# Optimization experiments

Hardware: AMD Instinct MI355X
Metric: run time of the kernel (lower is better)

Reference implementation:

```python
import jax, jax.numpy as jnp
import numpy as np

ALPHA, BETA, GAMMA = 1.0, 1.0, 0.7
WIN = 11
C1 = 0.01 ** 2
C2 = 0.03 ** 2


def get_sobel_kernels(n1=1, n2=2, n3=2):
    a = np.asarray
    Sx = a([[[-n1, 0, n1], [-n2, 0, n2], [-n1, 0, n1]],
            [[-n2, 0, n2], [-n3 * n2, 0, n3 * n2], [-n2, 0, n2]],
            [[-n1, 0, n1], [-n2, 0, n2], [-n1, 0, n1]]])
    Sy = a([[[-n1, -n2, -n1], [0, 0, 0], [n1, n2, n1]],
            [[-n2, -n3 * n2, -n2], [0, 0, 0], [n2, n3 * n2, n2]],
            [[-n1, -n2, -n1], [0, 0, 0], [n1, n2, n1]]])
    Sz = a([[[-n1, -n2, -n1], [-n2, -n3 * n2, -n2], [-n1, -n2, -n1]],
            [[0, 0, 0], [0, 0, 0], [0, 0, 0]],
            [[n1, n2, n1], [n2, n3 * n2, n2], [n1, n2, n1]]])
    Sd11 = a([[[0, n1, n2], [-n1, 0, n1], [-n2, -n1, 0]],
              [[0, n2, n2 * n3], [-n2, 0, n2], [-n2 * n3, -n2, 0]],
              [[0, n1, n2], [-n1, 0, n1], [-n2, -n1, 0]]])
    Sd12 = a([[[-n2, -n1, 0], [-n1, 0, n1], [0, n1, n2]],
              [[-n2 * n3, -n2, 0], [-n2, 0, n2], [0, n2, n2 * n3]],
              [[-n2, -n1, 0], [-n1, 0, n1], [0, n1, n2]]])
    Sd21 = Sd11.T
    Sd22 = Sd12.T
    Sd31 = a([-S.T for S in Sd11.T])
    Sd32 = a([S.T for S in Sd12.T])
    return np.stack([Sx, Sy, Sz, Sd11, Sd12, Sd21, Sd22, Sd31, Sd32]).astype(np.float32)

# (9,1,3,3,3) fused sobel bank -- single grouped conv instead of 9 launches
SOBEL_W = jnp.asarray(get_sobel_kernels()[:, None])


def _gauss1d():
    g = jnp.exp(-(jnp.arange(WIN, dtype=jnp.float32) - WIN // 2) ** 2 / (2 * 1.5 ** 2))
    return g / g.sum()

G1D = _gauss1d()


def conv3d(x, w):
    return jax.lax.conv_general_dilated(
        x, w, window_strides=(1, 1, 1), padding='SAME',
        dimension_numbers=('NCDHW', 'OIDHW', 'NCDHW'))


def gauss_filter(x):
    # separable 11-tap gaussian along D, H, W (== full 11^3 window, zero-padded SAME)
    x = conv3d(x, G1D.reshape(1, 1, WIN, 1, 1))
    x = conv3d(x, G1D.reshape(1, 1, 1, WIN, 1))
    x = conv3d(x, G1D.reshape(1, 1, 1, 1, WIN))
    return x


def edge_map(img):
    # GradEdge3D.__call__ with a=1, C=1
    B, C, D, H, W = img.shape
    xp = jnp.pad(img, ((0, 0), (0, 0), (1, 1), (1, 1), (1, 1)), mode='reflect')
    g = conv3d(xp, SOBEL_W)                       # (B, 9, D+2, H+2, W+2)
    gm = jnp.sqrt(jnp.sum((g + 1e-6) ** 2 + 1e-6, axis=1))  # (B, D+2, H+2, W+2)
    gm = gm[:, 1:-1, 1:-1, 1:-1]
    norm = (gm - gm.min()) / (gm.max() - gm.min() + 1e-6)
    return norm.reshape(B, 1, D, H, W)


def ssim_value(pred, target):
    mu_p = gauss_filter(pred)
    mu_t = gauss_filter(target)
    mu_p2, mu_t2, mu_pt = mu_p ** 2, mu_t ** 2, mu_p * mu_t
    sig_p = gauss_filter(pred * pred) - mu_p2
    sig_t = gauss_filter(target * target) - mu_t2
    sig_pt = gauss_filter(pred * target) - mu_pt
    ssim_map = ((2 * mu_pt + C1) * (2 * sig_pt + C2)) / ((mu_p2 + mu_t2 + C1) * (sig_p + sig_t + C2))
    return 1.0 - ssim_map.mean()


def setup_inputs() -> dict:
    key = jax.random.key(0)
    k1, k2 = jax.random.split(key)
    shape = (2, 1, 128, 128, 128)
    return {
        'pred': jax.random.uniform(k1, shape, dtype=jnp.float32),
        'target': jax.random.uniform(k2, shape, dtype=jnp.float32),
    }


def reference(pred, target):
    loss_mse = jnp.mean((pred - target) ** 2)
    loss_ssim = ssim_value(pred, target)
    # GMELoss3D: lam_errors=[(1.0, L1Loss())], reduction='sum'
    loss_gme = 1e-6 + jnp.mean(jnp.abs(edge_map(pred) - edge_map(target)))
    total = ALPHA * loss_mse + BETA * loss_ssim + GAMMA * loss_gme
    return (total, loss_mse, loss_ssim, loss_gme)
```

## Files before the change

### kernel.cpp

```cpp
#include <hip/hip_runtime.h>


#define VOL 4194304
#define HV  2097152

typedef _Float16 h2 __attribute__((ext_vector_type(2)));
typedef _Float16 h4 __attribute__((ext_vector_type(4)));
typedef _Float16 h8 __attribute__((ext_vector_type(8)));

constexpr float GW[11] = {
    0.00102838f, 0.00759876f, 0.03600077f, 0.10936070f, 0.21300554f,
    0.26601173f,
    0.21300554f, 0.10936070f, 0.03600077f, 0.00759876f, 0.00102838f};



__device__ __forceinline__ void wblur_body(
    const float* __restrict__ p, const float* __restrict__ t,
    _Float16* __restrict__ A, double* __restrict__ mseB, const int bidx,
    char* __restrict__ pool, float* __restrict__ redw) {
  float (* __restrict__ sr)[138] = (float (*)[138])pool;
  float (* __restrict__ dr)[138] = (float (*)[138])(pool + 8832);
  const int tid = threadIdx.x;
  const int gbase = bidx << 11;
  if (tid < 160) {
    const int r = tid / 10, j = tid % 10;
    const int c = (j < 5) ? j : (128 + j);
    sr[r][c] = 0.f; dr[r][c] = 0.f;
  }
  float msel = 0.f;
#pragma unroll
  for (int i = 0; i < 8; ++i) {
    const int v = (i << 8) + tid;
    const float pv = p[gbase + v];
    const float tv = t[gbase + v];
    const float sv = pv + tv, dv = pv - tv;
    sr[v >> 7][5 + (v & 127)] = sv;
    dr[v >> 7][5 + (v & 127)] = dv;
    msel += dv * dv;
  }
  __syncthreads();
  h4* __restrict__ A4 = (h4*)A;
#pragma unroll
  for (int i = 0; i < 8; ++i) {
    const int v = (i << 8) + tid;
    const int row = v >> 7, x = v & 127;
    float as = 0.f, ad = 0.f, ass = 0.f, add_ = 0.f;
#pragma unroll
    for (int k = 0; k < 11; ++k) {
      const float w = GW[k];
      const float a = sr[row][x + k];
      const float b = dr[row][x + k];
      const float wa = w * a;
      const float wb = w * b;
      as += wa; ad += wb;
      ass += wa * a; add_ += wb * b;
    }
    h4 o;
    o[0] = (_Float16)as;  o[1] = (_Float16)ad;
    o[2] = (_Float16)ass; o[3] = (_Float16)add_;
    A4[gbase + v] = o;
  }
  redw[tid] = msel;
  __syncthreads();
  for (int s = 128; s > 0; s >>= 1) {
    if (tid < s) redw[tid] += redw[tid + s];
    __syncthreads();
  }
  if (tid == 0) atomicAdd(&mseB[(bidx & 63) << 3], (double)redw[0]);
}

__device__ __forceinline__ void sobel_body(
    const float* __restrict__ p, const float* __restrict__ t,
    _Float16* __restrict__ gmP, _Float16* __restrict__ gmT,
    unsigned int* __restrict__ ui, const int bx, const int by, const int bz,
    char* __restrict__ pool, float* __restrict__ rmin) {
  float* __restrict__ sb   = (float*)pool;
  float* __restrict__ rmax = (float*)(pool + 5184);
  const int tid = threadIdx.x;
  const int tx = tid & 15;
  const int ty = tid >> 4;
  const int x0 = bx << 4;
  const int y0 = by << 4;
  const int vol = bz >> 3;
  const int b   = (bz >> 2) & 1;
  const int z0  = (bz & 3) << 5;
  const float* __restrict__ img = vol ? t : p;
  _Float16* __restrict__ gm = vol ? gmT : gmP;
  const int vb = b << 21;

  const int ly1 = tid / 24, lx1 = tid % 24;
  const bool v1 = (lx1 < 18);
  int gy1 = y0 - 1 + ly1; gy1 = gy1 < 0 ? 1 : (gy1 > 127 ? 126 : gy1);
  int gx1 = x0 - 1 + lx1; gx1 = gx1 < 0 ? 1 : (gx1 > 127 ? 126 : gx1);
  const int off1 = (gy1 << 7) + gx1;
  const int s2i = tid + 256;
  const int ly2 = s2i / 24, lx2 = s2i % 24;
  const bool v2 = (s2i < 432) && (lx2 < 18);
  int gy2 = y0 - 1 + ly2; gy2 = gy2 < 0 ? 1 : (gy2 > 127 ? 126 : gy2);
  int gx2 = x0 - 1 + lx2; gx2 = gx2 < 0 ? 1 : (gx2 > 127 ? 126 : gx2);
  const int off2 = (gy2 << 7) + gx2;
  const int rb = ty * 24 + tx;
  const int gbase = vb + (z0 << 14) + ((y0 + ty) << 7) + (x0 + tx);

  float Y0[7], Y1[7], Y2[7];
  float rv1 = 0.f, rv2 = 0.f;
  float lmin = 3.4e38f, lmax = 0.f;

#define LOADR(ZS) {                                                         \
    const int zc_ = (ZS) > 127 ? 126 : (ZS);                                \
    const int za_ = vb + (zc_ << 14);                                       \
    if (v1) rv1 = img[za_ + off1];                                          \
    if (v2) rv2 = img[za_ + off2]; }

#define WRITELDS(BOFF) {                                                    \
    if (v1) sb[(BOFF) + tid] = rv1;                                         \
    if (v2) sb[(BOFF) + s2i] = rv2; }

#define COMPY(P) {                                                          \
    const int o_ = (P) * 432 + rb;                                          \
    const float r00 = sb[o_],      r01 = sb[o_ + 1],  r02 = sb[o_ + 2];     \
    const float r10 = sb[o_ + 24], r11 = sb[o_ + 25], r12 = sb[o_ + 26];    \
    const float r20 = sb[o_ + 48], r21 = sb[o_ + 49], r22 = sb[o_ + 50];    \
    const float dx0 = r02 - r00, dx1 = r12 - r10, dx2 = r22 - r20;          \
    const float ux0 = r00 + r01 + r02, ux1 = r10 + r11 + r12,               \
                ux2 = r20 + r21 + r22;                                      \
    const float sx0 = ux0 + r01, sx1 = ux1 + r11, sx2 = ux2 + r21;          \
    Y##P[1] = dx0 + dx1 + dx2;                                    \
    Y##P[0] = Y##P[1] + dx1;                                      \
    Y##P[2] = sx2 - sx0;                                          \
    Y##P[4] = sx0 + sx1 + sx2;                                    \
    Y##P[3] = Y##P[4] + sx1;                                      \
    Y##P[5] = ux2 - ux0;                                          \
    Y##P[6] = (ux0 + ux2) + 2.f * ux1; }

#define EMIT(I, P0, P1, P2) {                                               \
    const float E_ = Y##P0[0] + Y##P1[0] + Y##P2[0];                        \
    const float g1 = E_ + Y##P1[0];                                         \
    const float tA = Y##P0[1] + Y##P1[1] + Y##P2[1];                        \
    const float A_ = tA + Y##P1[1];                                         \
    const float D_ = Y##P0[2] + Y##P1[2] + Y##P2[2];                        \
    const float g2 = D_ + Y##P1[2];                                         \
    const float g3 = Y##P2[3] - Y##P0[3];                                   \
    const float C_ = Y##P2[4] - Y##P0[4];                                   \
    const float B_ = (Y##P0[5] + Y##P2[5]) + 2.f * Y##P1[5];                \
    const float F_ = Y##P2[6] - Y##P0[6];                                   \
    const float g4 = A_ - B_, g5 = A_ + B_;                                 \
    const float g6 = C_ - D_, g7 = C_ + D_;                                 \
    const float g8 = E_ - F_, g9 = E_ + F_;                                 \
    float ss_ = 9e-6f, t_;                                                  \
    t_ = g1 + 1e-6f; ss_ = fmaf(t_, t_, ss_);                               \
    t_ = g2 + 1e-6f; ss_ = fmaf(t_, t_, ss_);                               \
    t_ = g3 + 1e-6f; ss_ = fmaf(t_, t_, ss_);                               \
    t_ = g4 + 1e-6f; ss_ = fmaf(t_, t_, ss_);                               \
    t_ = g5 + 1e-6f; ss_ = fmaf(t_, t_, ss_);                               \
    t_ = g6 + 1e-6f; ss_ = fmaf(t_, t_, ss_);                               \
    t_ = g7 + 1e-6f; ss_ = fmaf(t_, t_, ss_);                               \
    t_ = g8 + 1e-6f; ss_ = fmaf(t_, t_, ss_);                               \
    t_ = g9 + 1e-6f; ss_ = fmaf(t_, t_, ss_);                               \
    const _Float16 gh = (_Float16)sqrtf(ss_);                               \
    gm[gbase + ((I) << 14)] = gh;                                           \
    const float gq = (float)gh;                                             \
    lmin = fminf(lmin, gq); lmax = fmaxf(lmax, gq); }

#define BODY(I, P0, P1, P2) {                                               \
    WRITELDS((P2) * 432);                                                   \
    LOADR(z0 + (I) + 2);                                                    \
    __syncthreads();                                                        \
    COMPY(P2);                                                              \
    EMIT(I, P0, P1, P2); }

  {
    const int zp = (z0 == 0) ? 1 : (z0 - 1);
    LOADR(zp);  WRITELDS(0);
    LOADR(z0);  WRITELDS(432);
    __syncthreads();
    COMPY(0);
    COMPY(1);
    LOADR(z0 + 1);
  }
  for (int ii = 0; ii < 30; ii += 3) {
    BODY(ii,     0, 1, 2);
    BODY(ii + 1, 1, 2, 0);
    BODY(ii + 2, 2, 0, 1);
  }
  BODY(30, 0, 1, 2);
  BODY(31, 1, 2, 0);

#undef BODY
#undef EMIT
#undef COMPY
#undef WRITELDS
#undef LOADR

  rmin[tid] = lmin; rmax[tid] = lmax;
  __syncthreads();
  for (int st = 128; st > 0; st >>= 1) {
    if (tid < st) {
      rmin[tid] = fminf(rmin[tid], rmin[tid + st]);
      rmax[tid] = fmaxf(rmax[tid], rmax[tid + st]);
    }
    __syncthreads();
  }
  if (tid == 0) {
    const int bin = (bx + (by << 3) + (bz << 6)) & 63;
    atomicMax(&ui[vol * 1024 + (bin << 4)], ~__float_as_uint(rmin[0]));
    atomicMax(&ui[2048 + vol * 1024 + (bin << 4)], __float_as_uint(rmax[0]));
  }
}

__device__ __forceinline__ void blury_body(
    const _Float16* __restrict__ A, _Float16* __restrict__ B,
    const int z, const int yseg, const int batch) {
  __shared__ h8 s[26][64];
  const int tid = threadIdx.x;
  const int y0 = yseg << 4;
  const h8* __restrict__ Ah = (const h8*)A;
  h8* __restrict__ Bh = (h8*)B;
  const int slice8 = (batch << 20) + (z << 13);
  for (int l = tid; l < 1664; l += 256) {
    const int row = l >> 6, xc = l & 63;
    const int y = y0 - 5 + row;
    h8 v{};
    if ((unsigned)y < 128u) v = Ah[slice8 + (y << 6) + xc];
    s[row][xc] = v;
  }
  __syncthreads();
  const int xc = tid & 63;
  const int yg = tid >> 6;
#pragma unroll
  for (int r = 0; r < 4; ++r) {
    const int yo = (yg << 2) + r;
    h8 acc{};
#pragma unroll
    for (int k = 0; k < 11; ++k) {
      const _Float16 w = (_Float16)GW[k];
      acc += w * s[yo + k][xc];
    }
    Bh[slice8 + ((y0 + yo) << 6) + xc] = acc;
  }
}

__device__ __forceinline__ void edge_body(
    const _Float16* __restrict__ gmP, const _Float16* __restrict__ gmT,
    const unsigned int* __restrict__ ui, double* __restrict__ absB,
    const int bidx, float* __restrict__ rede) {
  unsigned umnp = 0u, umnt = 0u, umxp = 0u, umxt = 0u;
  for (int j = 0; j < 64; ++j) {
    const unsigned a0 = ui[j << 4];
    const unsigned a1 = ui[1024 + (j << 4)];
    const unsigned a2 = ui[2048 + (j << 4)];
    const unsigned a3 = ui[3072 + (j << 4)];
    umnp = umnp > a0 ? umnp : a0;
    umnt = umnt > a1 ? umnt : a1;
    umxp = umxp > a2 ? umxp : a2;
    umxt = umxt > a3 ? umxt : a3;
  }
  const float mnp = __uint_as_float(~umnp);
  const float mnt = __uint_as_float(~umnt);
  const float mxp = __uint_as_float(umxp);
  const float mxt = __uint_as_float(umxt);
  const float scp = 1.f / (mxp - mnp + 1e-6f);
  const float sct = 1.f / (mxt - mnt + 1e-6f);
  const h8* __restrict__ gp = (const h8*)gmP;
  const h8* __restrict__ gt = (const h8*)gmT;
  float lsum = 0.f;
  const int base = bidx << 9;
#pragma unroll
  for (int i = 0; i < 2; ++i) {
    const int idx = base + (i << 8) + threadIdx.x;
    const h8 a = gp[idx];
    const h8 b = gt[idx];
#pragma unroll
    for (int j = 0; j < 8; ++j)
      lsum += fabsf(((float)a[j] - mnp) * scp - ((float)b[j] - mnt) * sct);
  }
  rede[threadIdx.x] = lsum;
  __syncthreads();
  for (int s = 128; s > 0; s >>= 1) {
    if (threadIdx.x < s) rede[threadIdx.x] += rede[threadIdx.x + s];
    __syncthreads();
  }
  if (threadIdx.x == 0)
    atomicAdd(&absB[(bidx & 63) << 3], (double)rede[0]);
}

__global__ __launch_bounds__(256) void k_fused_a(
    const float* __restrict__ p, const float* __restrict__ t,
    _Float16* __restrict__ A, double* __restrict__ mseB,
    _Float16* __restrict__ gmP, _Float16* __restrict__ gmT,
    unsigned int* __restrict__ ui) {
  __shared__ __align__(16) char pool[17664];
  __shared__ float redshared[256];
  const int bid = blockIdx.x;
  const int r3 = bid % 3;
  if (r3 < 2) {
    wblur_body(p, t, A, mseB, (bid / 3) * 2 + r3, pool, redshared);
  } else {
    const int s = bid / 3;
    sobel_body(p, t, gmP, gmT, ui, s & 7, (s >> 3) & 7, s >> 6,
               pool, redshared);
  }
}

__global__ __launch_bounds__(256) void k_fused_b(
    const _Float16* __restrict__ A, _Float16* __restrict__ B) {
  const int idx = blockIdx.x;
  blury_body(A, B, idx & 127, (idx >> 7) & 7, idx >> 10);
}

__global__ __launch_bounds__(256) void k_zblur_ssim(
    const _Float16* __restrict__ B, double* __restrict__ ssimB,
    const _Float16* __restrict__ gmP, const _Float16* __restrict__ gmT,
    const unsigned int* __restrict__ ui, double* __restrict__ absB) {
  __shared__ h8 s[26][64];
  __shared__ float red[256];
  const int tid = threadIdx.x;
  const int bid = blockIdx.x;
  const int r3 = bid % 3;
  if (r3 == 2) {
    edge_body(gmP, gmT, ui, absB, bid / 3, red);
    return;
  }
  const int idx = (bid / 3) * 2 + r3;
  const int y = idx & 127;
  const int z0 = ((idx >> 7) & 7) << 4;
  const int batch = idx >> 10;
  const h8* __restrict__ Bh = (const h8*)B;
  const int col8 = (batch << 20) + (y << 6);
  for (int l = tid; l < 1664; l += 256) {
    const int row = l >> 6, xc = l & 63;
    const int zz = z0 - 5 + row;
    h8 v{};
    if ((unsigned)zz < 128u) v = Bh[col8 + (zz << 13) + xc];
    s[row][xc] = v;
  }
  __syncthreads();
  const int xc = tid & 63;
  const int zg = tid >> 6;
  float lsum = 0.f;
#pragma unroll
  for (int r = 0; r < 4; ++r) {
    const int zo = (zg << 2) + r;
    h8 m{};
#pragma unroll
    for (int k = 0; k < 11; ++k) {
      const _Float16 w = (_Float16)GW[k];
      m += w * s[zo + k][xc];
    }
#pragma unroll
    for (int j = 0; j < 2; ++j) {
      const float mus = (float)m[4 * j + 0];
      const float mud = (float)m[4 * j + 1];
      const float ess = (float)m[4 * j + 2];
      const float edd = (float)m[4 * j + 3];
      const float S2 = mus * mus, D2 = mud * mud;
      const float num = ((S2 - D2) * 0.5f + 1e-4f) *
                        ((ess - edd - S2 + D2) * 0.5f + 9e-4f);
      const float den = ((S2 + D2) * 0.5f + 1e-4f) *
                        ((ess + edd - S2 - D2) * 0.5f + 9e-4f);
      lsum += num / den;
    }
  }
  red[tid] = lsum;
  __syncthreads();
  for (int st = 128; st > 0; st >>= 1) {
    if (tid < st) red[tid] += red[tid + st];
    __syncthreads();
  }
  if (tid == 0) {
    const int bin = idx & 63;
    atomicAdd(&ssimB[bin << 3], (double)red[0]);
  }
}

__global__ void k_final(const double* __restrict__ dbl, float* __restrict__ out) {
  if (threadIdx.x == 0 && blockIdx.x == 0) {
    double ms = 0.0, ss = 0.0, ab = 0.0;
    for (int j = 0; j < 64; ++j) {
      ms += dbl[j << 3];
      ss += dbl[512 + (j << 3)];
      ab += dbl[1024 + (j << 3)];
    }
    const double N = 4194304.0;
    const double mse   = ms / N;
    const double ssiml = 1.0 - ss / N;
    const double gme   = 1e-6 + ab / N;
    const double total = mse + ssiml + 0.7 * gme;
    out[0] = (float)total;
    out[1] = (float)mse;
    out[2] = (float)ssiml;
    out[3] = (float)gme;
  }
}

extern "C" void kernel_launch(void* const* d_in, const int* in_sizes, int n_in,
                              void* d_out, int out_size, void* d_ws, size_t ws_size,
                              hipStream_t stream) {
  const float* p = (const float*)d_in[0];
  const float* t = (const float*)d_in[1];
  _Float16* A = (_Float16*)d_ws;
  _Float16* B = A + (size_t)4 * VOL;
  char* accb = (char*)d_ws + (size_t)20 * VOL;
  double* dbl = (double*)accb;
  unsigned int* ui = (unsigned int*)(accb + 12288);
  _Float16* gmP = (_Float16*)((char*)d_ws + 88080384);
  _Float16* gmT = gmP + VOL;
  float* out = (float*)d_out;

  hipMemsetAsync(accb, 0, 28672, stream);
  k_fused_a<<<3072, 256, 0, stream>>>(p, t, A, dbl, gmP, gmT, ui);
  k_fused_b<<<2048, 256, 0, stream>>>(A, B);
  k_zblur_ssim<<<3072, 256, 0, stream>>>(B, dbl + 512, gmP, gmT, ui, dbl + 1024);
  k_final<<<1, 64, 0, stream>>>(dbl, out);
}
```

Baseline: 149.4 us.

## Fuse Y-blur into X-blur kernel using shared-memory ring buffer

```diff
diff --git a/kernel.cpp b/kernel.cpp
--- a/kernel.cpp
+++ b/kernel.cpp
@@ -14,52 +14,81 @@
     0.21300554f, 0.10936070f, 0.03600077f, 0.00759876f, 0.00102838f};
 
 
-
-__device__ __forceinline__ void wblur_body(
+__device__ __forceinline__ void xyblur_body(
     const float* __restrict__ p, const float* __restrict__ t,
-    _Float16* __restrict__ A, double* __restrict__ mseB, const int bidx,
+    _Float16* __restrict__ A, double* __restrict__ mseB, const int xyidx,
     char* __restrict__ pool, float* __restrict__ redw) {
   float (* __restrict__ sr)[138] = (float (*)[138])pool;
   float (* __restrict__ dr)[138] = (float (*)[138])(pool + 8832);
+  h4 (* __restrict__ ring)[128]  = (h4 (*)[128])(pool + 17664);
   const int tid = threadIdx.x;
-  const int gbase = bidx << 11;
+  const int yhalf = xyidx & 1;
+  const int z = (xyidx >> 1) & 127;
+  const int b = xyidx >> 8;
+  const int ybase = yhalf << 6;
+  const int sbase = (b << 21) + (z << 14);
+  h4* __restrict__ A4 = (h4*)A;
   if (tid < 160) {
     const int r = tid / 10, j = tid % 10;
     const int c = (j < 5) ? j : (128 + j);
     sr[r][c] = 0.f; dr[r][c] = 0.f;
   }
   float msel = 0.f;
-#pragma unroll
-  for (int i = 0; i < 8; ++i) {
-    const int v = (i << 8) + tid;
-    const float pv = p[gbase + v];
-    const float tv = t[gbase + v];
-    const float sv = pv + tv, dv = pv - tv;
-    sr[v >> 7][5 + (v & 127)] = sv;
-    dr[v >> 7][5 + (v & 127)] = dv;
-    msel += dv * dv;
-  }
-  __syncthreads();
-  h4* __restrict__ A4 = (h4*)A;
-#pragma unroll
-  for (int i = 0; i < 8; ++i) {
-    const int v = (i << 8) + tid;
-    const int row = v >> 7, x = v & 127;
-    float as = 0.f, ad = 0.f, ass = 0.f, add_ = 0.f;
-#pragma unroll
-    for (int k = 0; k < 11; ++k) {
-      const float w = GW[k];
-      const float a = sr[row][x + k];
-      const float b = dr[row][x + k];
-      const float wa = w * a;
-      const float wb = w * b;
-      as += wa; ad += wb;
-      ass += wa * a; add_ += wb * b;
-    }
-    h4 o;
-    o[0] = (_Float16)as;  o[1] = (_Float16)ad;
-    o[2] = (_Float16)ass; o[3] = (_Float16)add_;
-    A4[gbase + v] = o;
+  for (int j = 0; j < 5; ++j) {
+    const int c0 = ybase - 5 + (j << 4);
+#pragma unroll
+    for (int i = 0; i < 8; ++i) {
+      const int v = (i << 8) + tid;
+      const int rr = v >> 7, x = v & 127;
+      const int gy = c0 + rr;
+      float sv = 0.f, dv = 0.f;
+      if ((unsigned)gy < 128u) {
+        const float pv = p[sbase + (gy << 7) + x];
+        const float tv = t[sbase + (gy << 7) + x];
+        sv = pv + tv; dv = pv - tv;
+        if (gy >= ybase && gy <= ybase + 63) msel += dv * dv;
+      }
+      sr[rr][5 + x] = sv;
+      dr[rr][5 + x] = dv;
+    }
+    __syncthreads();
+#pragma unroll
+    for (int i = 0; i < 8; ++i) {
+      const int v = (i << 8) + tid;
+      const int rr = v >> 7, x = v & 127;
+      float as = 0.f, ad = 0.f, ass = 0.f, add_ = 0.f;
+#pragma unroll
+      for (int k = 0; k < 11; ++k) {
+        const float w = GW[k];
+        const float a = sr[rr][x + k];
+        const float bb = dr[rr][x + k];
+        const float wa = w * a;
+        const float wb = w * bb;
+        as += wa; ad += wb;
+        ass += wa * a; add_ += wb * bb;
+      }
+      h4 o;
+      o[0] = (_Float16)as;  o[1] = (_Float16)ad;
+      o[2] = (_Float16)ass; o[3] = (_Float16)add_;
+      ring[(c0 + rr) & 31][x] = o;
+    }
+    __syncthreads();
+#pragma unroll
+    for (int i = 0; i < 8; ++i) {
+      const int v = (i << 8) + tid;
+      const int er = c0 - 5 + (v >> 7);
+      const int x = v & 127;
+      if (er >= ybase && er <= ybase + 63) {
+        h4 acc{};
+#pragma unroll
+        for (int k = 0; k < 11; ++k) {
+          const _Float16 w = (_Float16)GW[k];
+          acc += w * ring[(er - 5 + k) & 31][x];
+        }
+        A4[sbase + (er << 7) + x] = acc;
+      }
+    }
+    __syncthreads();
   }
   redw[tid] = msel;
   __syncthreads();
@@ -67,7 +96,7 @@
     if (tid < s) redw[tid] += redw[tid + s];
     __syncthreads();
   }
-  if (tid == 0) atomicAdd(&mseB[(bidx & 63) << 3], (double)redw[0]);
+  if (tid == 0) atomicAdd(&mseB[(xyidx & 63) << 3], (double)redw[0]);
 }
 
 __device__ __forceinline__ void sobel_body(
@@ -209,38 +238,6 @@
   }
 }
 
-__device__ __forceinline__ void blury_body(
-    const _Float16* __restrict__ A, _Float16* __restrict__ B,
-    const int z, const int yseg, const int batch) {
-  __shared__ h8 s[26][64];
-  const int tid = threadIdx.x;
-  const int y0 = yseg << 4;
-  const h8* __restrict__ Ah = (const h8*)A;
-  h8* __restrict__ Bh = (h8*)B;
-  const int slice8 = (batch << 20) + (z << 13);
-  for (int l = tid; l < 1664; l += 256) {
-    const int row = l >> 6, xc = l & 63;
-    const int y = y0 - 5 + row;
-    h8 v{};
-    if ((unsigned)y < 128u) v = Ah[slice8 + (y << 6) + xc];
-    s[row][xc] = v;
-  }
-  __syncthreads();
-  const int xc = tid & 63;
-  const int yg = tid >> 6;
-#pragma unroll
-  for (int r = 0; r < 4; ++r) {
-    const int yo = (yg << 2) + r;
-    h8 acc{};
-#pragma unroll
-    for (int k = 0; k < 11; ++k) {
-      const _Float16 w = (_Float16)GW[k];
-      acc += w * s[yo + k][xc];
-    }
-    Bh[slice8 + ((y0 + yo) << 6) + xc] = acc;
-  }
-}
-
 __device__ __forceinline__ void edge_body(
     const _Float16* __restrict__ gmP, const _Float16* __restrict__ gmT,
     const unsigned int* __restrict__ ui, double* __restrict__ absB,
@@ -290,27 +287,21 @@
     _Float16* __restrict__ A, double* __restrict__ mseB,
     _Float16* __restrict__ gmP, _Float16* __restrict__ gmT,
     unsigned int* __restrict__ ui) {
-  __shared__ __align__(16) char pool[17664];
+  __shared__ __align__(16) char pool[50432];
   __shared__ float redshared[256];
   const int bid = blockIdx.x;
   const int r3 = bid % 3;
-  if (r3 < 2) {
-    wblur_body(p, t, A, mseB, (bid / 3) * 2 + r3, pool, redshared);
+  if (r3 == 0) {
+    xyblur_body(p, t, A, mseB, bid / 3, pool, redshared);
   } else {
-    const int s = bid / 3;
+    const int s = (bid / 3) * 2 + (r3 - 1);
     sobel_body(p, t, gmP, gmT, ui, s & 7, (s >> 3) & 7, s >> 6,
                pool, redshared);
   }
 }
 
-__global__ __launch_bounds__(256) void k_fused_b(
-    const _Float16* __restrict__ A, _Float16* __restrict__ B) {
-  const int idx = blockIdx.x;
-  blury_body(A, B, idx & 127, (idx >> 7) & 7, idx >> 10);
-}
-
 __global__ __launch_bounds__(256) void k_zblur_ssim(
-    const _Float16* __restrict__ B, double* __restrict__ ssimB,
+    const _Float16* __restrict__ A, double* __restrict__ ssimB,
     const _Float16* __restrict__ gmP, const _Float16* __restrict__ gmT,
     const unsigned int* __restrict__ ui, double* __restrict__ absB) {
   __shared__ h8 s[26][64];
@@ -326,13 +317,13 @@
   const int y = idx & 127;
   const int z0 = ((idx >> 7) & 7) << 4;
   const int batch = idx >> 10;
-  const h8* __restrict__ Bh = (const h8*)B;
+  const h8* __restrict__ Ah = (const h8*)A;
   const int col8 = (batch << 20) + (y << 6);
   for (int l = tid; l < 1664; l += 256) {
     const int row = l >> 6, xc = l & 63;
     const int zz = z0 - 5 + row;
     h8 v{};
-    if ((unsigned)zz < 128u) v = Bh[col8 + (zz << 13) + xc];
+    if ((unsigned)zz < 128u) v = Ah[col8 + (zz << 13) + xc];
     s[row][xc] = v;
   }
   __syncthreads();
@@ -400,7 +391,6 @@
   const float* p = (const float*)d_in[0];
   const float* t = (const float*)d_in[1];
   _Float16* A = (_Float16*)d_ws;
-  _Float16* B = A + (size_t)4 * VOL;
   char* accb = (char*)d_ws + (size_t)20 * VOL;
   double* dbl = (double*)accb;
   unsigned int* ui = (unsigned int*)(accb + 12288);
@@ -409,8 +399,7 @@
   float* out = (float*)d_out;
 
   hipMemsetAsync(accb, 0, 28672, stream);
-  k_fused_a<<<3072, 256, 0, stream>>>(p, t, A, dbl, gmP, gmT, ui);
-  k_fused_b<<<2048, 256, 0, stream>>>(A, B);
-  k_zblur_ssim<<<3072, 256, 0, stream>>>(B, dbl + 512, gmP, gmT, ui, dbl + 1024);
+  k_fused_a<<<1536, 256, 0, stream>>>(p, t, A, dbl, gmP, gmT, ui);
+  k_zblur_ssim<<<3072, 256, 0, stream>>>(A, dbl + 512, gmP, gmT, ui, dbl + 1024);
   k_final<<<1, 64, 0, stream>>>(dbl, out);
 }
```

Result: slower. 162.1 us (+8.5%).
